# Optimization experiments

Hardware: AMD Instinct MI355X
Metric: run time of the kernel (lower is better)

Reference implementation:

```python
import jax, jax.numpy as jnp
import numpy as np

NUM_BOND_TYPE = 6
NUM_BOND_DIRECTION = 3
HIDDEN = 128
OUT = 128


def setup_inputs() -> dict:
    key = jax.random.key(0)
    ks = jax.random.split(key, 12)
    N, E = 50000, 800000
    x = jax.random.normal(ks[0], (N, HIDDEN), dtype=jnp.float32)
    edge_index = jax.random.randint(ks[1], (2, E), 0, N, dtype=jnp.int64 if jax.config.jax_enable_x64 else jnp.int32)
    edge_attr = jax.random.randint(ks[2], (E, 2), 0, 3, dtype=edge_index.dtype)
    mask_node_indices = jax.random.randint(ks[3], (5000,), 0, N, dtype=edge_index.dtype)
    s = 1.0 / np.sqrt(HIDDEN)
    W_enc = jax.random.uniform(ks[4], (HIDDEN, HIDDEN), jnp.float32, -s, s)  # enc_to_dec, no bias
    W1 = jax.random.uniform(ks[5], (2 * HIDDEN, HIDDEN), jnp.float32, -s, s)
    b1 = jax.random.uniform(ks[6], (2 * HIDDEN,), jnp.float32, -s, s)
    s2 = 1.0 / np.sqrt(2 * HIDDEN)
    W2 = jax.random.uniform(ks[7], (OUT, 2 * HIDDEN), jnp.float32, -s2, s2)
    b2 = jax.random.uniform(ks[8], (OUT,), jnp.float32, -s2, s2)
    # xavier_uniform for embeddings
    g1 = np.sqrt(6.0 / (NUM_BOND_TYPE + HIDDEN))
    g2 = np.sqrt(6.0 / (NUM_BOND_DIRECTION + HIDDEN))
    emb1 = jax.random.uniform(ks[9], (NUM_BOND_TYPE, HIDDEN), jnp.float32, -g1, g1)
    emb2 = jax.random.uniform(ks[10], (NUM_BOND_DIRECTION, HIDDEN), jnp.float32, -g2, g2)
    prelu_a = jnp.array(0.25, dtype=jnp.float32)
    return {"x": x, "edge_index": edge_index, "edge_attr": edge_attr,
            "mask_node_indices": mask_node_indices, "prelu_a": prelu_a,
            "W_enc": W_enc, "W1": W1, "b1": b1, "W2": W2, "b2": b2,
            "emb1": emb1, "emb2": emb2}


def reference(x, edge_index, edge_attr, mask_node_indices, prelu_a,
              W_enc, W1, b1, W2, b2, emb1, emb2):
    N = x.shape[0]
    # PReLU activation then enc_to_dec linear (no bias)
    h = jnp.where(x > 0, x, prelu_a * x)
    h = h @ W_enc.T
    # zero out masked nodes
    h = h.at[mask_node_indices].set(0.0)
    # add self loops
    loops = jnp.arange(N, dtype=edge_index.dtype)
    src = jnp.concatenate([edge_index[0], loops])
    dst = jnp.concatenate([edge_index[1], loops])
    # self-loop edge_attr: [4, 0]
    sl_attr = jnp.concatenate([jnp.full((N, 1), 4, dtype=edge_attr.dtype),
                               jnp.zeros((N, 1), dtype=edge_attr.dtype)], axis=1)
    ea = jnp.concatenate([edge_attr, sl_attr], axis=0)
    edge_emb = emb1[ea[:, 0]] + emb2[ea[:, 1]]  # [E+N, H]
    # message: x_j + edge_attr, aggregate (add) at target nodes
    msg = h[src] + edge_emb
    aggr = jax.ops.segment_sum(msg, dst, num_segments=N)  # [N, H]
    # GIN update MLP: H -> 2H -> OUT
    out = jax.nn.relu(aggr @ W1.T + b1) @ W2.T + b2
    return out
```

## Files before the change

### kernel.cpp

```cpp
#include <hip/hip_runtime.h>

#define HID 128
#define HID2 256
#define NBMAX 3200
#define STRIDE 384

typedef __attribute__((ext_vector_type(8))) short bf16x8;
typedef __attribute__((ext_vector_type(4))) float f32x4;

__device__ inline ushort f2b(float f) {
    union { float f; unsigned u; } v; v.f = f;
    unsigned r = v.u + 0x7FFF + ((v.u >> 16) & 1);
    return (ushort)(r >> 16);
}
__device__ inline float b2f(unsigned hi16) {
    union { unsigned u; float f; } v; v.u = hi16 << 16;
    return v.f;
}

#define SZ0 (HID * HID)
#define SZ1 (HID2 * HID)
#define SZ2 (HID * HID2)

__global__ __launch_bounds__(256) void k_prep(const float* __restrict__ w0,
                                              const float* __restrict__ w1,
                                              const float* __restrict__ w2,
                                              const float* __restrict__ e1,
                                              const float* __restrict__ e2,
                                              const int* __restrict__ midx,
                                              ushort* __restrict__ o0,
                                              ushort* __restrict__ o1,
                                              ushort* __restrict__ o2,
                                              ushort* __restrict__ comboT,
                                              int* __restrict__ gcursor,
                                              int* __restrict__ maskbits, int M) {
    const int t = threadIdx.x;
    if (blockIdx.x == gridDim.x - 1) {
        for (int j = t; j < 2048; j += 256) maskbits[j] = 0;
        __syncthreads();
        for (int j = t; j < M; j += 256) {
            int r = midx[j];
            atomicOr(&maskbits[r >> 5], 1 << (r & 31));
        }
        return;
    }
    int i = blockIdx.x * 256 + t;
    if (i < SZ0) { o0[i] = f2b(w0[i]); return; }
    i -= SZ0;
    if (i < SZ1) { o1[i] = f2b(w1[i]); return; }
    i -= SZ1;
    if (i < SZ2) { o2[i] = f2b(w2[i]); return; }
    i -= SZ2;
    if (i < 4096) {
        int col = i >> 5, tt = i & 31;
        float v = 0.f;
        if (tt < 18) v = e1[(tt / 3) * HID + col] + e2[(tt % 3) * HID + col];
        comboT[col * 32 + tt] = f2b(v);
        return;
    }
    i -= 4096;
    if (i < 4096) gcursor[i] = i * STRIDE;
}

__global__ __launch_bounds__(256) void k_prelu(const float* __restrict__ x,
                                               const float* __restrict__ pa,
                                               const int* __restrict__ maskbits,
                                               ushort* __restrict__ p, int total8) {
    int i = blockIdx.x * 256 + threadIdx.x;
    if (i >= total8) return;
    int row = i >> 4;
    if ((maskbits[row >> 5] >> (row & 31)) & 1) {
        ushort z[8] = {0,0,0,0,0,0,0,0};
        *(bf16x8*)(p + (size_t)i * 8) = *(bf16x8*)z;
        return;
    }
    const float a = pa[0];
    float4 v0 = *(const float4*)(x + (size_t)i * 8);
    float4 v1 = *(const float4*)(x + (size_t)i * 8 + 4);
    float vv[8] = {v0.x, v0.y, v0.z, v0.w, v1.x, v1.y, v1.z, v1.w};
    ushort u[8];
#pragma unroll
    for (int j = 0; j < 8; ++j) {
        float f = vv[j] > 0.f ? vv[j] : a * vv[j];
        u[j] = f2b(f);
    }
    *(bf16x8*)(p + (size_t)i * 8) = *(bf16x8*)u;
}

__global__ __launch_bounds__(256) void k_bscat(const int* __restrict__ src,
                                               const int* __restrict__ dst,
                                               const int* __restrict__ ea,
                                               int* __restrict__ gcursor,
                                               unsigned* __restrict__ bucketed,
                                               int E, int nbuck) {
    __shared__ int lh[NBMAX];
    __shared__ int gbs[NBMAX];
    const int t = threadIdx.x;
    const int base = blockIdx.x * 4096;
    for (int i = t; i < nbuck; i += 256) lh[i] = 0;
    __syncthreads();
    unsigned keys[16];
    int bk[16];
    int rk[16];
#pragma unroll
    for (int j = 0; j < 16; ++j) {
        int e = base + j * 256 + t;
        bk[j] = -1;
        if (e < E) {
            int d = dst[e];
            int cm = ea[2 * e] * 3 + ea[2 * e + 1];
            keys[j] = (unsigned)src[e] | ((unsigned)(d & 15) << 16) | ((unsigned)cm << 20);
            bk[j] = d >> 4;
            rk[j] = atomicAdd(&lh[bk[j]], 1);
        }
    }
    __syncthreads();
    for (int i = t; i < nbuck; i += 256) gbs[i] = lh[i] ? atomicAdd(&gcursor[i], lh[i]) : 0;
    __syncthreads();
#pragma unroll
    for (int j = 0; j < 16; ++j)
        if (bk[j] >= 0) {
            int pos = gbs[bk[j]] + rk[j];
            int lim = (bk[j] + 1) * STRIDE;
            if (pos < lim) bucketed[pos] = keys[j];
        }
}

__global__ __launch_bounds__(512) void k_baccum3(const ushort* __restrict__ p,
                                                 const int* __restrict__ gcursor,
                                                 const unsigned* __restrict__ bucketed,
                                                 ushort* __restrict__ A,
                                                 ushort* __restrict__ A2, int N) {
    __shared__ unsigned skeys[STRIDE];
    __shared__ int cnt[16];
    __shared__ int soff[16];
    __shared__ int cur[16];
    __shared__ int cnts[16][18];
    const int t = threadIdx.x;
    const int n0 = blockIdx.x << 4;
    const int w = t >> 6, l = t & 63;
    const int g = l >> 4, c16 = l & 15;

    for (int i = t; i < 16 * 18; i += 512) cnts[i / 18][i % 18] = ((i % 18) == 12) ? 1 : 0;

    float acc[2][8];
#pragma unroll
    for (int nn = 0; nn < 2; ++nn) {
        int gn = n0 + w * 2 + nn;
        uint4 pv = {0u, 0u, 0u, 0u};
        if (g == 0 && gn < N) pv = *(const uint4*)(p + (size_t)gn * HID + c16 * 8);
#pragma unroll
        for (int q = 0; q < 4; ++q) {
            unsigned u = (&pv.x)[q];
            acc[nn][2 * q]     = (g == 0) ? b2f(u & 0xffffu) : 0.f;
            acc[nn][2 * q + 1] = (g == 0) ? b2f(u >> 16) : 0.f;
        }
    }

    const int s0 = blockIdx.x * STRIDE;
    const int m = gcursor[blockIdx.x] - s0;
    if (t < 16) cnt[t] = 0;
    __syncthreads();
    if (t < m) atomicAdd(&cnt[(bucketed[s0 + t] >> 16) & 15], 1);
    __syncthreads();
    if (t < 16) {
        int v = cnt[t];
        int sc = v;
#pragma unroll
        for (int o = 1; o < 16; o <<= 1) {
            int u = __shfl_up(sc, o, 64);
            if (t >= o) sc += u;
        }
        soff[t] = sc - v;
        cur[t] = sc - v;
    }
    __syncthreads();
    if (t < m) {
        unsigned key = bucketed[s0 + t];
        int dl = (key >> 16) & 15;
        int r = atomicAdd(&cur[dl], 1);
        skeys[r] = key;
        atomicAdd(&cnts[dl][key >> 20], 1);
    }
    __syncthreads();
#pragma unroll
    for (int nn = 0; nn < 2; ++nn) {
        const int node = w * 2 + nn;
        const int eb = soff[node];
        const int c = cnt[node];
        for (int k = 0; k < c; k += 16) {
            int iA = k + g, iB = k + 4 + g, iC = k + 8 + g, iD = k + 12 + g;
            bool vA = iA < c, vB = iB < c, vC = iC < c, vD = iD < c;
            unsigned keyA = skeys[eb + (vA ? iA : c - 1)];
            unsigned keyB = skeys[eb + (vB ? iB : c - 1)];
            unsigned keyC = skeys[eb + (vC ? iC : c - 1)];
            unsigned keyD = skeys[eb + (vD ? iD : c - 1)];
            uint4 pa4 = *(const uint4*)(p + (size_t)(keyA & 0xffffu) * HID + c16 * 8);
            uint4 pb4 = *(const uint4*)(p + (size_t)(keyB & 0xffffu) * HID + c16 * 8);
            uint4 pc4 = *(const uint4*)(p + (size_t)(keyC & 0xffffu) * HID + c16 * 8);
            uint4 pd4 = *(const uint4*)(p + (size_t)(keyD & 0xffffu) * HID + c16 * 8);
#pragma unroll
            for (int q = 0; q < 4; ++q) {
                unsigned ua = (&pa4.x)[q], ub = (&pb4.x)[q];
                unsigned uc = (&pc4.x)[q], ud = (&pd4.x)[q];
                float s0f = (vA ? b2f(ua & 0xffffu) : 0.f) + (vB ? b2f(ub & 0xffffu) : 0.f)
                          + (vC ? b2f(uc & 0xffffu) : 0.f) + (vD ? b2f(ud & 0xffffu) : 0.f);
                float s1f = (vA ? b2f(ua >> 16) : 0.f) + (vB ? b2f(ub >> 16) : 0.f)
                          + (vC ? b2f(uc >> 16) : 0.f) + (vD ? b2f(ud >> 16) : 0.f);
                acc[nn][2 * q]     += s0f;
                acc[nn][2 * q + 1] += s1f;
            }
        }
    }
#pragma unroll
    for (int nn = 0; nn < 2; ++nn) {
        int gn = n0 + w * 2 + nn;
        unsigned ou[4];
#pragma unroll
        for (int q = 0; q < 4; ++q) {
            float v0 = acc[nn][2 * q], v1 = acc[nn][2 * q + 1];
            v0 += __shfl_xor(v0, 16, 64); v1 += __shfl_xor(v1, 16, 64);
            v0 += __shfl_xor(v0, 32, 64); v1 += __shfl_xor(v1, 32, 64);
            ou[q] = (unsigned)f2b(v0) | ((unsigned)f2b(v1) << 16);
        }
        if (g == 0 && gn < N)
            *(uint4*)(A + (size_t)gn * HID + c16 * 8) = *(uint4*)ou;
    }
    __syncthreads();
    if (t < 16 * 16) {
        int r = t >> 4, cp = t & 15;
        int gn = n0 + r;
        if (gn < N) {
            int i0 = 2 * cp, i1 = 2 * cp + 1;
            ushort u0 = (i0 < 18) ? f2b((float)cnts[r][i0]) : (ushort)0;
            ushort u1 = (i1 < 18) ? f2b((float)cnts[r][i1]) : (ushort)0;
            *(unsigned*)(A2 + (size_t)gn * 32 + 2 * cp) = (unsigned)u0 | ((unsigned)u1 << 16);
        }
    }
}

__global__ __launch_bounds__(512, 8) void k_fused(const ushort* __restrict__ A,
                                                  const ushort* __restrict__ A2,
                                                  const ushort* __restrict__ Wencb,
                                                  const ushort* __restrict__ comboT,
                                                  const ushort* __restrict__ W1b,
                                                  const float* __restrict__ b1,
                                                  const ushort* __restrict__ W2b,
                                                  const float* __restrict__ b2,
                                                  float* __restrict__ out, int N) {
    __shared__ char smem[53248];
    const int t = threadIdx.x;
    const int bn = blockIdx.x * 64;
    {
        int seg = t & 15, r0 = t >> 4;
#pragma unroll
        for (int i = 0; i < 2; ++i) {
            int row = r0 + i * 32;
            int grow = bn + row;
            bf16x8 v;
            if (grow < N) v = *(const bf16x8*)(A + (size_t)grow * HID + seg * 8);
            else { ushort z[8] = {0,0,0,0,0,0,0,0}; v = *(bf16x8*)z; }
            *(bf16x8*)(smem + row * 256 + ((seg * 16) ^ ((row & 7) << 4))) = v;
        }
    }
    if (t < 256) {
        int row = t >> 2, seg = t & 3;
        int grow = bn + row;
        bf16x8 v;
        if (grow < N) v = *(const bf16x8*)(A2 + (size_t)grow * 32 + seg * 8);
        else { ushort z[8] = {0,0,0,0,0,0,0,0}; v = *(bf16x8*)z; }
        *(bf16x8*)(smem + 16384 + row * 64 + ((seg * 16) ^ ((row & 3) << 4))) = v;
    }
    __syncthreads();
    const int w = t >> 6, l = t & 63;
    const int lrow = l & 15, lk = l >> 4;
    {
        const int n = w * 16 + lrow;
        bf16x8 wf[4], cf;
#pragma unroll
        for (int ks = 0; ks < 4; ++ks)
            wf[ks] = *(const bf16x8*)(Wencb + n * HID + ks * 32 + lk * 8);
        cf = *(const bf16x8*)(comboT + n * 32 + lk * 8);
#pragma unroll
        for (int rt = 0; rt < 4; ++rt) {
            int arow = rt * 16 + lrow;
            bf16x8 af[4], a2f;
#pragma unroll
            for (int ks = 0; ks < 4; ++ks)
                af[ks] = *(const bf16x8*)(smem + arow * 256 + ((ks * 64 + lk * 16) ^ ((arow & 7) << 4)));
            a2f = *(const bf16x8*)(smem + 16384 + arow * 64 + ((lk * 16) ^ ((arow & 3) << 4)));
            f32x4 acc = {0.f, 0.f, 0.f, 0.f};
#pragma unroll
            for (int ks = 0; ks < 4; ++ks)
                acc = __builtin_amdgcn_mfma_f32_16x16x32_bf16(af[ks], wf[ks], acc, 0, 0, 0);
            acc = __builtin_amdgcn_mfma_f32_16x16x32_bf16(a2f, cf, acc, 0, 0, 0);
#pragma unroll
            for (int r = 0; r < 4; ++r) {
                int row2 = rt * 16 + lk * 4 + r;
                *(ushort*)(smem + 20480 + row2 * 256 + ((2 * n) ^ ((row2 & 7) << 4))) = f2b(acc[r]);
            }
        }
    }
    __syncthreads();
    for (int j = 0; j < 2; ++j) {
        const int n = (2 * w + j) * 16 + lrow;
        bf16x8 wf[4];
#pragma unroll
        for (int ks = 0; ks < 4; ++ks)
            wf[ks] = *(const bf16x8*)(W1b + n * HID + ks * 32 + lk * 8);
        const float bb = b1[n];
        const int h2base = (w < 4) ? 0 : 36864;
        const int cl = (2 * w + j) * 16 + lrow - ((w < 4) ? 0 : 128);
#pragma unroll
        for (int rt = 0; rt < 4; ++rt) {
            int arow = rt * 16 + lrow;
            bf16x8 hf[4];
#pragma unroll
            for (int ks = 0; ks < 4; ++ks)
                hf[ks] = *(const bf16x8*)(smem + 20480 + arow * 256 + ((ks * 64 + lk * 16) ^ ((arow & 7) << 4)));
            f32x4 acc = {0.f, 0.f, 0.f, 0.f};
#pragma unroll
            for (int ks = 0; ks < 4; ++ks)
                acc = __builtin_amdgcn_mfma_f32_16x16x32_bf16(hf[ks], wf[ks], acc, 0, 0, 0);
#pragma unroll
            for (int r = 0; r < 4; ++r) {
                float v = acc[r] + bb;
                v = v > 0.f ? v : 0.f;
                int row2 = rt * 16 + lk * 4 + r;
                *(ushort*)(smem + h2base + row2 * 256 + ((2 * cl) ^ ((row2 & 7) << 4))) = f2b(v);
            }
        }
    }
    __syncthreads();
    {
        const int n = w * 16 + lrow;
        const float bb = b2[n];
#pragma unroll
        for (int rt = 0; rt < 4; ++rt) {
            int arow = rt * 16 + lrow;
            f32x4 acc = {0.f, 0.f, 0.f, 0.f};
            {
                bf16x8 gf[4], wf[4];
#pragma unroll
                for (int ks = 0; ks < 4; ++ks) {
                    gf[ks] = *(const bf16x8*)(smem + arow * 256 + ((ks * 64 + lk * 16) ^ ((arow & 7) << 4)));
                    wf[ks] = *(const bf16x8*)(W2b + n * HID2 + ks * 32 + lk * 8);
                }
#pragma unroll
                for (int ks = 0; ks < 4; ++ks)
                    acc = __builtin_amdgcn_mfma_f32_16x16x32_bf16(gf[ks], wf[ks], acc, 0, 0, 0);
            }
            {
                bf16x8 gf[4], wf[4];
#pragma unroll
                for (int ks = 0; ks < 4; ++ks) {
                    gf[ks] = *(const bf16x8*)(smem + 36864 + arow * 256 + ((ks * 64 + lk * 16) ^ ((arow & 7) << 4)));
                    wf[ks] = *(const bf16x8*)(W2b + n * HID2 + (ks + 4) * 32 + lk * 8);
                }
#pragma unroll
                for (int ks = 0; ks < 4; ++ks)
                    acc = __builtin_amdgcn_mfma_f32_16x16x32_bf16(gf[ks], wf[ks], acc, 0, 0, 0);
            }
#pragma unroll
            for (int r = 0; r < 4; ++r) {
                int grow = bn + rt * 16 + lk * 4 + r;
                if (grow < N) out[(size_t)grow * HID + n] = acc[r] + bb;
            }
        }
    }
}

extern "C" void kernel_launch(void* const* d_in, const int* in_sizes, int n_in,
                              void* d_out, int out_size, void* d_ws, size_t ws_size,
                              hipStream_t stream) {
    const float* x     = (const float*)d_in[0];
    const int*   eidx  = (const int*)d_in[1];
    const int*   eattr = (const int*)d_in[2];
    const int*   mask  = (const int*)d_in[3];
    const float* pa    = (const float*)d_in[4];
    const float* Wenc  = (const float*)d_in[5];
    const float* W1    = (const float*)d_in[6];
    const float* b1    = (const float*)d_in[7];
    const float* W2    = (const float*)d_in[8];
    const float* b2    = (const float*)d_in[9];
    const float* emb1  = (const float*)d_in[10];
    const float* emb2  = (const float*)d_in[11];

    const int N = in_sizes[0] / HID;
    const int E = in_sizes[1] / 2;
    const int M = in_sizes[3];

    const int* src = eidx;
    const int* dst = eidx + E;

    const int nbuck = (N + 15) >> 4;

    ushort*   p        = (ushort*)d_ws;
    ushort*   A        = p + (size_t)N * HID;
    ushort*   A2       = A + (size_t)N * HID;
    ushort*   Wencb    = A2 + (size_t)N * 32;
    ushort*   W1b      = Wencb + SZ0;
    ushort*   W2b      = W1b + SZ1;
    ushort*   comboT   = W2b + SZ2;
    int*      gcursor  = (int*)(comboT + 4096);
    int*      maskbits = gcursor + 4096;
    unsigned* bucketed = (unsigned*)(maskbits + 2048);

    const int nb64 = (N + 63) / 64;
    const int total8 = N * HID / 8;
    const int nbE = (E + 4095) / 4096;
    const int prepTotal = SZ0 + SZ1 + SZ2 + 4096 + 4096;

    k_prep<<<(prepTotal + 255) / 256 + 1, 256, 0, stream>>>(Wenc, W1, W2, emb1, emb2, mask,
                                                            Wencb, W1b, W2b, comboT, gcursor,
                                                            maskbits, M);
    k_prelu<<<(total8 + 255) / 256, 256, 0, stream>>>(x, pa, maskbits, p, total8);
    k_bscat<<<nbE, 256, 0, stream>>>(src, dst, eattr, gcursor, bucketed, E, nbuck);
    k_baccum3<<<nbuck, 512, 0, stream>>>(p, gcursor, bucketed, A, A2, N);
    k_fused<<<nb64, 512, 0, stream>>>(A, A2, Wencb, comboT, W1b, b1, W2b, b2, (float*)d_out, N);
}
```

Before: 101.8 us.

## Fuse bucketed edge aggregation into the MLP kernel via shared memory

Merges the aggregation kernel and the fused GEMM/MLP kernel into one kernel. Each 64-node block aggregates its four 16-node buckets and writes the bf16 aggregates and edge-type count rows straight into the swizzled shared-memory tiles the GEMM stage reads. This removes the global write and re-read of the A and A2 intermediates and one kernel launch. In exchange, blocks become 4x coarser (fewer blocks, serial loop over buckets), and occupancy is capped by shared-memory usage and a lower launch-bounds hint.

Result: slower. 108.3 us (+6.4%).

```diff
diff --git a/kernel.cpp b/kernel.cpp
--- a/kernel.cpp
+++ b/kernel.cpp
@@ -126,48 +126,51 @@
         }
 }
 
-__global__ __launch_bounds__(512) void k_baccum3(const ushort* __restrict__ p,
+__global__ __launch_bounds__(512, 6) void k_mega(const ushort* __restrict__ p,
                                                  const int* __restrict__ gcursor,
                                                  const unsigned* __restrict__ bucketed,
-                                                 ushort* __restrict__ A,
-                                                 ushort* __restrict__ A2, int N) {
-    __shared__ unsigned skeys[STRIDE];
-    __shared__ int cnt[16];
-    __shared__ int soff[16];
-    __shared__ int cur[16];
-    __shared__ int cnts[16][18];
+                                                 const ushort* __restrict__ Wencb,
+                                                 const ushort* __restrict__ comboT,
+                                                 const ushort* __restrict__ W1b,
+                                                 const float* __restrict__ b1,
+                                                 const ushort* __restrict__ W2b,
+                                                 const float* __restrict__ b2,
+                                                 float* __restrict__ out, int N) {
+    __shared__ char smem[53248];
+    unsigned* skeys = (unsigned*)(smem + 20480);
+    int* cnt  = (int*)(smem + 26624);
+    int* soff = (int*)(smem + 26880);
+    int* cur  = (int*)(smem + 27136);
+    int (*cnts)[18] = (int(*)[18])(smem + 27392);
     const int t = threadIdx.x;
-    const int n0 = blockIdx.x << 4;
     const int w = t >> 6, l = t & 63;
     const int g = l >> 4, c16 = l & 15;
-
-    for (int i = t; i < 16 * 18; i += 512) cnts[i / 18][i % 18] = ((i % 18) == 12) ? 1 : 0;
-
-    float acc[2][8];
-#pragma unroll
-    for (int nn = 0; nn < 2; ++nn) {
-        int gn = n0 + w * 2 + nn;
-        uint4 pv = {0u, 0u, 0u, 0u};
-        if (g == 0 && gn < N) pv = *(const uint4*)(p + (size_t)gn * HID + c16 * 8);
-#pragma unroll
-        for (int q = 0; q < 4; ++q) {
-            unsigned u = (&pv.x)[q];
-            acc[nn][2 * q]     = (g == 0) ? b2f(u & 0xffffu) : 0.f;
-            acc[nn][2 * q + 1] = (g == 0) ? b2f(u >> 16) : 0.f;
-        }
-    }
-
-    const int s0 = blockIdx.x * STRIDE;
-    const int m = gcursor[blockIdx.x] - s0;
-    if (t < 16) cnt[t] = 0;
-    __syncthreads();
-    if (t < m) atomicAdd(&cnt[(bucketed[s0 + t] >> 16) & 15], 1);
-    __syncthreads();
-    if (t < 16) {
+    const int bn = blockIdx.x * 64;
+    const int b0 = blockIdx.x * 4;
+
+    int mr[4];
+#pragma unroll
+    for (int r = 0; r < 4; ++r) {
+        int v = gcursor[b0 + r] - (b0 + r) * STRIDE;
+        mr[r] = v < 0 ? 0 : (v > STRIDE ? STRIDE : v);
+    }
+
+    for (int i = t; i < 64 * 18; i += 512) cnts[i / 18][i % 18] = ((i % 18) == 12) ? 1 : 0;
+    if (t < 64) cnt[t] = 0;
+    __syncthreads();
+    for (int j = t; j < 1536; j += 512) {
+        int r = j / 384, i = j % 384;
+        if (i < mr[r]) {
+            unsigned key = bucketed[(size_t)(b0 + r) * STRIDE + i];
+            atomicAdd(&cnt[r * 16 + ((key >> 16) & 15)], 1);
+        }
+    }
+    __syncthreads();
+    if (t < 64) {
         int v = cnt[t];
         int sc = v;
 #pragma unroll
-        for (int o = 1; o < 16; o <<= 1) {
+        for (int o = 1; o < 64; o <<= 1) {
             int u = __shfl_up(sc, o, 64);
             if (t >= o) sc += u;
         }
@@ -175,104 +178,85 @@
         cur[t] = sc - v;
     }
     __syncthreads();
-    if (t < m) {
-        unsigned key = bucketed[s0 + t];
-        int dl = (key >> 16) & 15;
-        int r = atomicAdd(&cur[dl], 1);
-        skeys[r] = key;
-        atomicAdd(&cnts[dl][key >> 20], 1);
-    }
-    __syncthreads();
-#pragma unroll
-    for (int nn = 0; nn < 2; ++nn) {
-        const int node = w * 2 + nn;
-        const int eb = soff[node];
-        const int c = cnt[node];
-        for (int k = 0; k < c; k += 16) {
-            int iA = k + g, iB = k + 4 + g, iC = k + 8 + g, iD = k + 12 + g;
-            bool vA = iA < c, vB = iB < c, vC = iC < c, vD = iD < c;
-            unsigned keyA = skeys[eb + (vA ? iA : c - 1)];
-            unsigned keyB = skeys[eb + (vB ? iB : c - 1)];
-            unsigned keyC = skeys[eb + (vC ? iC : c - 1)];
-            unsigned keyD = skeys[eb + (vD ? iD : c - 1)];
-            uint4 pa4 = *(const uint4*)(p + (size_t)(keyA & 0xffffu) * HID + c16 * 8);
-            uint4 pb4 = *(const uint4*)(p + (size_t)(keyB & 0xffffu) * HID + c16 * 8);
-            uint4 pc4 = *(const uint4*)(p + (size_t)(keyC & 0xffffu) * HID + c16 * 8);
-            uint4 pd4 = *(const uint4*)(p + (size_t)(keyD & 0xffffu) * HID + c16 * 8);
-#pragma unroll
-            for (int q = 0; q < 4; ++q) {
-                unsigned ua = (&pa4.x)[q], ub = (&pb4.x)[q];
-                unsigned uc = (&pc4.x)[q], ud = (&pd4.x)[q];
-                float s0f = (vA ? b2f(ua & 0xffffu) : 0.f) + (vB ? b2f(ub & 0xffffu) : 0.f)
-                          + (vC ? b2f(uc & 0xffffu) : 0.f) + (vD ? b2f(ud & 0xffffu) : 0.f);
-                float s1f = (vA ? b2f(ua >> 16) : 0.f) + (vB ? b2f(ub >> 16) : 0.f)
-                          + (vC ? b2f(uc >> 16) : 0.f) + (vD ? b2f(ud >> 16) : 0.f);
-                acc[nn][2 * q]     += s0f;
-                acc[nn][2 * q + 1] += s1f;
-            }
-        }
-    }
-#pragma unroll
-    for (int nn = 0; nn < 2; ++nn) {
-        int gn = n0 + w * 2 + nn;
-        unsigned ou[4];
-#pragma unroll
-        for (int q = 0; q < 4; ++q) {
-            float v0 = acc[nn][2 * q], v1 = acc[nn][2 * q + 1];
-            v0 += __shfl_xor(v0, 16, 64); v1 += __shfl_xor(v1, 16, 64);
-            v0 += __shfl_xor(v0, 32, 64); v1 += __shfl_xor(v1, 32, 64);
-            ou[q] = (unsigned)f2b(v0) | ((unsigned)f2b(v1) << 16);
-        }
-        if (g == 0 && gn < N)
-            *(uint4*)(A + (size_t)gn * HID + c16 * 8) = *(uint4*)ou;
-    }
-    __syncthreads();
-    if (t < 16 * 16) {
-        int r = t >> 4, cp = t & 15;
-        int gn = n0 + r;
-        if (gn < N) {
-            int i0 = 2 * cp, i1 = 2 * cp + 1;
-            ushort u0 = (i0 < 18) ? f2b((float)cnts[r][i0]) : (ushort)0;
-            ushort u1 = (i1 < 18) ? f2b((float)cnts[r][i1]) : (ushort)0;
-            *(unsigned*)(A2 + (size_t)gn * 32 + 2 * cp) = (unsigned)u0 | ((unsigned)u1 << 16);
-        }
-    }
-}
-
-__global__ __launch_bounds__(512, 8) void k_fused(const ushort* __restrict__ A,
-                                                  const ushort* __restrict__ A2,
-                                                  const ushort* __restrict__ Wencb,
-                                                  const ushort* __restrict__ comboT,
-                                                  const ushort* __restrict__ W1b,
-                                                  const float* __restrict__ b1,
-                                                  const ushort* __restrict__ W2b,
-                                                  const float* __restrict__ b2,
-                                                  float* __restrict__ out, int N) {
-    __shared__ char smem[53248];
-    const int t = threadIdx.x;
-    const int bn = blockIdx.x * 64;
-    {
-        int seg = t & 15, r0 = t >> 4;
-#pragma unroll
-        for (int i = 0; i < 2; ++i) {
-            int row = r0 + i * 32;
-            int grow = bn + row;
-            bf16x8 v;
-            if (grow < N) v = *(const bf16x8*)(A + (size_t)grow * HID + seg * 8);
-            else { ushort z[8] = {0,0,0,0,0,0,0,0}; v = *(bf16x8*)z; }
-            *(bf16x8*)(smem + row * 256 + ((seg * 16) ^ ((row & 7) << 4))) = v;
-        }
-    }
-    if (t < 256) {
-        int row = t >> 2, seg = t & 3;
-        int grow = bn + row;
-        bf16x8 v;
-        if (grow < N) v = *(const bf16x8*)(A2 + (size_t)grow * 32 + seg * 8);
-        else { ushort z[8] = {0,0,0,0,0,0,0,0}; v = *(bf16x8*)z; }
-        *(bf16x8*)(smem + 16384 + row * 64 + ((seg * 16) ^ ((row & 3) << 4))) = v;
-    }
-    __syncthreads();
-    const int w = t >> 6, l = t & 63;
+    for (int j = t; j < 1536; j += 512) {
+        int r = j / 384, i = j % 384;
+        if (i < mr[r]) {
+            unsigned key = bucketed[(size_t)(b0 + r) * STRIDE + i];
+            int node = r * 16 + ((key >> 16) & 15);
+            int rk = atomicAdd(&cur[node], 1);
+            skeys[rk] = key;
+            atomicAdd(&cnts[node][key >> 20], 1);
+        }
+    }
+    __syncthreads();
+    for (int i = t; i < 64 * 16; i += 512) {
+        int r = i >> 4, cp = i & 15;
+        int i0 = 2 * cp, i1 = 2 * cp + 1;
+        ushort u0 = (i0 < 18) ? f2b((float)cnts[r][i0]) : (ushort)0;
+        ushort u1 = (i1 < 18) ? f2b((float)cnts[r][i1]) : (ushort)0;
+        *(unsigned*)(smem + 16384 + r * 64 + ((4 * cp) ^ ((r & 3) << 4))) =
+            (unsigned)u0 | ((unsigned)u1 << 16);
+    }
+    for (int q = 0; q < 4; ++q) {
+        float acc[2][8];
+#pragma unroll
+        for (int nn = 0; nn < 2; ++nn) {
+            int lr = q * 16 + w * 2 + nn;
+            int gn = bn + lr;
+            uint4 pv = {0u, 0u, 0u, 0u};
+            if (g == 0 && gn < N) pv = *(const uint4*)(p + (size_t)gn * HID + c16 * 8);
+#pragma unroll
+            for (int qq = 0; qq < 4; ++qq) {
+                unsigned u = (&pv.x)[qq];
+                acc[nn][2 * qq]     = (g == 0) ? b2f(u & 0xffffu) : 0.f;
+                acc[nn][2 * qq + 1] = (g == 0) ? b2f(u >> 16) : 0.f;
+            }
+        }
+#pragma unroll
+        for (int nn = 0; nn < 2; ++nn) {
+            const int node = q * 16 + w * 2 + nn;
+            const int eb = soff[node];
+            const int c = cnt[node];
+            for (int k = 0; k < c; k += 16) {
+                int iA = k + g, iB = k + 4 + g, iC = k + 8 + g, iD = k + 12 + g;
+                bool vA = iA < c, vB = iB < c, vC = iC < c, vD = iD < c;
+                unsigned keyA = skeys[eb + (vA ? iA : c - 1)];
+                unsigned keyB = skeys[eb + (vB ? iB : c - 1)];
+                unsigned keyC = skeys[eb + (vC ? iC : c - 1)];
+                unsigned keyD = skeys[eb + (vD ? iD : c - 1)];
+                uint4 pa4 = *(const uint4*)(p + (size_t)(keyA & 0xffffu) * HID + c16 * 8);
+                uint4 pb4 = *(const uint4*)(p + (size_t)(keyB & 0xffffu) * HID + c16 * 8);
+                uint4 pc4 = *(const uint4*)(p + (size_t)(keyC & 0xffffu) * HID + c16 * 8);
+                uint4 pd4 = *(const uint4*)(p + (size_t)(keyD & 0xffffu) * HID + c16 * 8);
+#pragma unroll
+                for (int qq = 0; qq < 4; ++qq) {
+                    unsigned ua = (&pa4.x)[qq], ub = (&pb4.x)[qq];
+                    unsigned uc = (&pc4.x)[qq], ud = (&pd4.x)[qq];
+                    float s0f = (vA ? b2f(ua & 0xffffu) : 0.f) + (vB ? b2f(ub & 0xffffu) : 0.f)
+                              + (vC ? b2f(uc & 0xffffu) : 0.f) + (vD ? b2f(ud & 0xffffu) : 0.f);
+                    float s1f = (vA ? b2f(ua >> 16) : 0.f) + (vB ? b2f(ub >> 16) : 0.f)
+                              + (vC ? b2f(uc >> 16) : 0.f) + (vD ? b2f(ud >> 16) : 0.f);
+                    acc[nn][2 * qq]     += s0f;
+                    acc[nn][2 * qq + 1] += s1f;
+                }
+            }
+        }
+#pragma unroll
+        for (int nn = 0; nn < 2; ++nn) {
+            int lr = q * 16 + w * 2 + nn;
+            unsigned ou[4];
+#pragma unroll
+            for (int qq = 0; qq < 4; ++qq) {
+                float v0 = acc[nn][2 * qq], v1 = acc[nn][2 * qq + 1];
+                v0 += __shfl_xor(v0, 16, 64); v1 += __shfl_xor(v1, 16, 64);
+                v0 += __shfl_xor(v0, 32, 64); v1 += __shfl_xor(v1, 32, 64);
+                ou[qq] = (unsigned)f2b(v0) | ((unsigned)f2b(v1) << 16);
+            }
+            if (g == 0)
+                *(uint4*)(smem + lr * 256 + ((c16 * 16) ^ ((lr & 7) << 4))) = *(uint4*)ou;
+        }
+    }
+    __syncthreads();
     const int lrow = l & 15, lk = l >> 4;
     {
         const int n = w * 16 + lrow;
@@ -396,9 +380,7 @@
     const int nbuck = (N + 15) >> 4;
 
     ushort*   p        = (ushort*)d_ws;
-    ushort*   A        = p + (size_t)N * HID;
-    ushort*   A2       = A + (size_t)N * HID;
-    ushort*   Wencb    = A2 + (size_t)N * 32;
+    ushort*   Wencb    = p + (size_t)N * HID;
     ushort*   W1b      = Wencb + SZ0;
     ushort*   W2b      = W1b + SZ1;
     ushort*   comboT   = W2b + SZ2;
@@ -416,6 +398,6 @@
                                                             maskbits, M);
     k_prelu<<<(total8 + 255) / 256, 256, 0, stream>>>(x, pa, maskbits, p, total8);
     k_bscat<<<nbE, 256, 0, stream>>>(src, dst, eattr, gcursor, bucketed, E, nbuck);
-    k_baccum3<<<nbuck, 512, 0, stream>>>(p, gcursor, bucketed, A, A2, N);
-    k_fused<<<nb64, 512, 0, stream>>>(A, A2, Wencb, comboT, W1b, b1, W2b, b2, (float*)d_out, N);
-}
+    k_mega<<<nb64, 512, 0, stream>>>(p, gcursor, bucketed, Wencb, comboT, W1b, b1, W2b, b2,
+                                     (float*)d_out, N);
+}
```
